# Performance work log

Measured on AMD Instinct MI355X. Metric: run time of the kernel, lower is better.

The kernel has to match this reference:

```python
import jax, jax.numpy as jnp
import numpy as np

BITS = 4
IN_F = 4096
OUT_F = 4096
NUMVALS = 200000
TOPX = 10
B, S = 4, 2048


def setup_inputs() -> dict:
    key = jax.random.key(0)
    ks = jax.random.split(key, 9)
    x = jax.random.normal(ks[0], (B, S, IN_F), dtype=jnp.float32)
    qweight = jax.random.randint(ks[1], (IN_F // 32 * BITS, OUT_F),
                                 jnp.iinfo(jnp.int32).min, jnp.iinfo(jnp.int32).max,
                                 dtype=jnp.int32)
    lookup_table = jax.random.normal(ks[2], (OUT_F, 2 ** BITS), dtype=jnp.float32) * 0.02
    bias = jax.random.normal(ks[3], (OUT_F,), dtype=jnp.float32) * 0.01
    rows = jnp.sort(jax.random.randint(ks[4], (OUT_F + 1,), 0, NUMVALS, dtype=jnp.int32))
    rows = rows.at[0].set(0).at[-1].set(NUMVALS)  # valid CSR row pointers
    cols = jax.random.randint(ks[5], (NUMVALS,), 0, IN_F, dtype=jnp.int32)
    vals = jax.random.normal(ks[6], (NUMVALS,), dtype=jnp.float32) * 0.02
    full_rows = jax.random.normal(ks[7], (IN_F, TOPX), dtype=jnp.float32) * 0.02
    full_row_indices = (jnp.arange(TOPX, dtype=jnp.int32) * (OUT_F // TOPX))
    return {"x": x, "qweight": qweight, "lookup_table": lookup_table, "bias": bias,
            "rows": rows, "cols": cols, "vals": vals,
            "full_rows": full_rows, "full_row_indices": full_row_indices}


def _dequant(qweight, lookup_table):
    # unpack 4-bit codes packed along infeatures into each int32 word
    per_word = 32 // BITS
    shifts = (jnp.arange(per_word, dtype=jnp.int32) * BITS)
    codes = (qweight[:, None, :] >> shifts[None, :, None]) & ((1 << BITS) - 1)
    codes = codes.reshape(-1, qweight.shape[1])  # (IN_F, OUT_F)
    # per-output-channel LUT gather: W[i, j] = lut[j, codes[i, j]]
    return jnp.take_along_axis(lookup_table.T, codes, axis=0)  # (IN_F, OUT_F)


def reference(x, qweight, lookup_table, bias, rows, cols, vals, full_rows, full_row_indices):
    w = _dequant(qweight, lookup_table)  # (IN_F, OUT_F) float32
    # CSR sparse outlier correction (row pointers over output channels)
    nnz = vals.shape[0]
    row_ids = jnp.searchsorted(rows, jnp.arange(nnz, dtype=jnp.int32), side="right") - 1
    w = w.at[cols, row_ids].add(vals)
    # topX dense outlier channels
    w = w.at[:, full_row_indices].add(full_rows)
    tokens = x.reshape(-1, x.shape[-1])  # (B*S, IN_F)
    y = tokens @ w + bias
    return y.reshape(x.shape[:-1] + (w.shape[1],))
```

## Files before the change

### kernel.cpp

```cpp
#include <hip/hip_runtime.h>
#include <hip/hip_bf16.h>
#include <stdint.h>

#define IN_F 4096
#define OUT_F 4096
#define MTOK 8192
#define TOPX_N 10
#define NUMVALS 200000
#define CSR_BLOCKS ((NUMVALS + 255) / 256)
#define CVT_BLOCKS ((MTOK * IN_F / 8) / 256)

typedef __bf16 bf16x8 __attribute__((ext_vector_type(8)));
typedef float f32x4 __attribute__((ext_vector_type(4)));

__device__ __forceinline__ void gld_lds16(const void* g, void* l) {
    __builtin_amdgcn_global_load_lds((const __attribute__((address_space(1))) void*)g,
                                     (__attribute__((address_space(3))) void*)l, 16, 0, 0);
}

__global__ __launch_bounds__(256) void k_dequant(const int* __restrict__ qw,
                                                 const float* __restrict__ lut,
                                                 __bf16* __restrict__ Wt) {
    __shared__ int qs[64 * 65];
    __shared__ float ls[64 * 16];
    const int b = blockIdx.x;
    const int jc = (b & 63) * 64;
    const int wc = (b >> 6) * 64;
    const int t = threadIdx.x;

    {
        float4 v = *(const float4*)(lut + (size_t)(jc + (t >> 2)) * 16 + (t & 3) * 4);
        *(float4*)(ls + (t >> 2) * 16 + (t & 3) * 4) = v;
    }
#pragma unroll
    for (int p = 0; p < 4; ++p) {
        int idx = t + p * 256;
        int row = idx >> 4;
        int c4 = (idx & 15) * 4;
        int4 v = *(const int4*)(qw + (size_t)(wc + row) * OUT_F + jc + c4);
        int base = row * 65 + c4;
        qs[base] = v.x; qs[base + 1] = v.y; qs[base + 2] = v.z; qs[base + 3] = v.w;
    }
    __syncthreads();

    const int wave = t >> 6, lane = t & 63;
#pragma unroll
    for (int i = 0; i < 16; ++i) {
        const int c = wave * 16 + i;
        const unsigned q = (unsigned)qs[lane * 65 + c];
        const float* lp = ls + c * 16;
        bf16x8 v;
#pragma unroll
        for (int e = 0; e < 8; ++e) v[e] = (__bf16)lp[(q >> (4 * e)) & 15];
        *(bf16x8*)(Wt + (size_t)(jc + c) * IN_F + (size_t)(wc + lane) * 8) = v;
    }
}

__device__ __forceinline__ void bf16_cas_add(__bf16* Wt, size_t elem, float v) {
    unsigned* wp = (unsigned*)Wt + (elem >> 1);
    unsigned sh = (unsigned)(elem & 1) * 16;
    unsigned old = *wp, assumed;
    do {
        assumed = old;
        union { unsigned u; float f; } cv;
        cv.u = ((assumed >> sh) & 0xFFFFu) << 16;
        __bf16 nb = (__bf16)(cv.f + v);
        unsigned nh = *(unsigned short*)&nb;
        unsigned newv = (assumed & ~(0xFFFFu << sh)) | ((unsigned)nh << sh);
        old = atomicCAS(wp, assumed, newv);
    } while (old != assumed);
}

__global__ __launch_bounds__(256) void k_prep(const float* __restrict__ x,
                                              __bf16* __restrict__ xb,
                                              const int* __restrict__ rows,
                                              const int* __restrict__ cols,
                                              const float* __restrict__ vals,
                                              const float* __restrict__ fr,
                                              const int* __restrict__ fri,
                                              __bf16* __restrict__ Wt) {
    const int b = blockIdx.x;
    if (b < CVT_BLOCKS) {
        size_t t = (size_t)b * 256 + threadIdx.x;
        const float4* p = (const float4*)x + 2 * t;
        float4 a = p[0], c = p[1];
        bf16x8 v;
        v[0] = (__bf16)a.x; v[1] = (__bf16)a.y; v[2] = (__bf16)a.z; v[3] = (__bf16)a.w;
        v[4] = (__bf16)c.x; v[5] = (__bf16)c.y; v[6] = (__bf16)c.z; v[7] = (__bf16)c.w;
        ((bf16x8*)xb)[t] = v;
    } else if (b < CVT_BLOCKS + CSR_BLOCKS) {
        int n = (b - CVT_BLOCKS) * 256 + threadIdx.x;
        if (n >= NUMVALS) return;
        int lo = 0, hi = OUT_F + 1;
        while (lo < hi) {
            int mid = (lo + hi) >> 1;
            if (rows[mid] <= n) lo = mid + 1; else hi = mid;
        }
        int r = lo - 1;
        bf16_cas_add(Wt, (size_t)r * IN_F + cols[n], vals[n]);
    } else {
        int i = (b - CVT_BLOCKS - CSR_BLOCKS) * 256 + threadIdx.x;
        if (i >= IN_F) return;
#pragma unroll
        for (int t = 0; t < TOPX_N; ++t) {
            int j = fri[t];
            bf16_cas_add(Wt, (size_t)j * IN_F + i, fr[(size_t)i * TOPX_N + t]);
        }
    }
}

#define BK_G 32
#define NKT (IN_F / BK_G)
#define TILE_BYTES 16384
#define MFMA_ __builtin_amdgcn_mfma_f32_16x16x32_bf16

__global__ __launch_bounds__(512, 2) void k_gemm(const __bf16* __restrict__ A,
                                                 const __bf16* __restrict__ Bt,
                                                 const float* __restrict__ bias,
                                                 float* __restrict__ C) {
    __shared__ __align__(1024) char smem[4][2][TILE_BYTES];

    const int tid = threadIdx.x;
    const int wave = tid >> 6, lane = tid & 63;
    const int wm = wave >> 2, wn = wave & 3;

    const int bid = blockIdx.x;
    const int swz = (bid & 7) * 64 + (bid >> 3);
    const int n0 = (swz & 15) * 256;
    const int m0 = (swz >> 4) * 256;

    const int q = lane & 7, g = (lane >> 3) & 3, rh = lane >> 5;
    const int rloc = ((5 * (q - g + 8)) & 7) + 8 * rh;
    const int w0 = wave * 2;

    const char* gA0 = (const char*)(A  + (size_t)(m0 + w0 * 16 + rloc) * IN_F) + g * 16;
    const char* gA1 = gA0 + 16 * IN_F * 2;
    const char* gB0 = (const char*)(Bt + (size_t)(n0 + w0 * 16 + rloc) * IN_F) + g * 16;
    const char* gB1 = gB0 + 16 * IN_F * 2;
    char* lA = (char*)smem[0][0] + w0 * 1024;
    char* lB = (char*)smem[0][1] + w0 * 1024;

    const int lrow = lane & 15, kk = lane >> 4;
    const int rdc = ((5 * lrow + kk) & 7) * 16 + kk * 128 + (lrow >> 3) * 512;
    const int rdA = wm * 8192 + rdc;
    const int rdB = wn * 4096 + rdc;

#define STAGE(boff, koff) do {                               \
        gld_lds16(gA0 + (koff), lA + (boff));                \
        gld_lds16(gA1 + (koff), lA + (boff) + 1024);         \
        gld_lds16(gB0 + (koff), lB + (boff));                \
        gld_lds16(gB1 + (koff), lB + (boff) + 1024);         \
    } while (0)

#define COMPUTE(boff) do {                                                                     \
        const char* pA = (const char*)smem[0][0] + (boff) + rdA;                               \
        const char* pB = (const char*)smem[0][1] + (boff) + rdB;                               \
        bf16x8 bfr[4], af0[4], af1[4];                                                         \
        _Pragma("unroll") for (int n = 0; n < 4; ++n) bfr[n] = *(const bf16x8*)(pB + n * 1024);\
        _Pragma("unroll") for (int m = 0; m < 4; ++m) af0[m] = *(const bf16x8*)(pA + m * 1024);\
        _Pragma("unroll") for (int m = 0; m < 4; ++m) af1[m] = *(const bf16x8*)(pA + 4096 + m * 1024);\
        __builtin_amdgcn_s_setprio(1);                                                         \
        _Pragma("unroll") for (int m = 0; m < 4; ++m)                                          \
            _Pragma("unroll") for (int n = 0; n < 4; ++n)                                      \
                acc[m][n] = MFMA_(af0[m], bfr[n], acc[m][n], 0, 0, 0);                         \
        _Pragma("unroll") for (int m = 0; m < 4; ++m)                                          \
            _Pragma("unroll") for (int n = 0; n < 4; ++n)                                      \
                acc[m + 4][n] = MFMA_(af1[m], bfr[n], acc[m + 4][n], 0, 0, 0);                 \
        __builtin_amdgcn_s_setprio(0);                                                         \
    } while (0)

    f32x4 acc[8][4] = {};

    STAGE(0, 0);
    STAGE(32768, 64);
    STAGE(65536, 128);

    int cboff = 0, sboff = 98304;
    for (int t = 0; t < NKT - 2; ++t) {
        asm volatile("s_waitcnt vmcnt(8)" ::: "memory");
        __builtin_amdgcn_s_barrier();
        asm volatile("" ::: "memory");
        if (t + 3 < NKT) STAGE(sboff, (t + 3) * 64);
        COMPUTE(cboff);
        cboff = cboff == 98304 ? 0 : cboff + 32768;
        sboff = sboff == 98304 ? 0 : sboff + 32768;
    }
    asm volatile("s_waitcnt vmcnt(4)" ::: "memory");
    __builtin_amdgcn_s_barrier();
    asm volatile("" ::: "memory");
    COMPUTE(cboff);
    cboff = cboff == 98304 ? 0 : cboff + 32768;
    asm volatile("s_waitcnt vmcnt(0)" ::: "memory");
    __builtin_amdgcn_s_barrier();
    asm volatile("" ::: "memory");
    COMPUTE(cboff);

    const int m0w = m0 + wm * 128;
    const int n0w = n0 + wn * 64;
#pragma unroll
    for (int n = 0; n < 4; ++n) {
        const int col = n0w + n * 16 + lrow;
        const float bj = bias[col];
#pragma unroll
        for (int m = 0; m < 8; ++m) {
            const int row = m0w + m * 16 + kk * 4;
#pragma unroll
            for (int r = 0; r < 4; ++r)
                C[(size_t)(row + r) * OUT_F + col] = acc[m][n][r] + bj;
        }
    }
#undef STAGE
#undef COMPUTE
}

extern "C" void kernel_launch(void* const* d_in, const int* in_sizes, int n_in,
                              void* d_out, int out_size, void* d_ws, size_t ws_size,
                              hipStream_t stream) {
    const float* x         = (const float*)d_in[0];
    const int*   qweight   = (const int*)d_in[1];
    const float* lut       = (const float*)d_in[2];
    const float* bias      = (const float*)d_in[3];
    const int*   rows      = (const int*)d_in[4];
    const int*   cols      = (const int*)d_in[5];
    const float* vals      = (const float*)d_in[6];
    const float* full_rows = (const float*)d_in[7];
    const int*   fri       = (const int*)d_in[8];
    float* out = (float*)d_out;

    __bf16* Wt = (__bf16*)d_ws;
    __bf16* xb = (__bf16*)((char*)d_ws + (size_t)OUT_F * IN_F * 2);

    k_dequant<<<dim3(64 * 8), 256, 0, stream>>>(qweight, lut, Wt);
    k_prep<<<dim3(CVT_BLOCKS + CSR_BLOCKS + IN_F / 256), 256, 0, stream>>>(
        x, xb, rows, cols, vals, full_rows, fri, Wt);
    k_gemm<<<dim3((OUT_F / 256) * (MTOK / 256)), 512, 0, stream>>>(xb, Wt, bias, out);
}
```

Measured before the change: 533.4 us.

## Double-buffer LDS fragment reads in registers to overlap with MFMA compute

Restructures the GEMM main loop into a software-pipelined ping-pong: the LDS fragment reads for the next k-tile go into a second register set while MFMAs run on the current set. Scheduling barriers pin this order. The loop is manually unrolled by two with explicit waitcnt and barrier placement, and the tail is rewritten. The aim is to hide LDS read latency behind matrix math, at the cost of doubling the fragment registers, which may pressure occupancy at two blocks per CU.

```diff
diff --git a/kernel.cpp b/kernel.cpp
--- a/kernel.cpp
+++ b/kernel.cpp
@@ -113,12 +113,18 @@
 #define NKT (IN_F / BK_G)
 #define TILE_BYTES 16384
 #define MFMA_ __builtin_amdgcn_mfma_f32_16x16x32_bf16
+#define SB0 __builtin_amdgcn_sched_barrier(0)
+#define VMC4  asm volatile("s_waitcnt vmcnt(4)" ::: "memory")
+#define VMC0  asm volatile("s_waitcnt vmcnt(0)" ::: "memory")
+#define BARF  do { __builtin_amdgcn_s_barrier(); asm volatile("" ::: "memory"); } while (0)
+#define ROT(x) ((x) == 98304 ? 0 : (x) + 32768)
 
 __global__ __launch_bounds__(512, 2) void k_gemm(const __bf16* __restrict__ A,
                                                  const __bf16* __restrict__ Bt,
                                                  const float* __restrict__ bias,
                                                  float* __restrict__ C) {
     __shared__ __align__(1024) char smem[4][2][TILE_BYTES];
+    char* const sm = (char*)smem;
 
     const int tid = threadIdx.x;
     const int wave = tid >> 6, lane = tid & 63;
@@ -143,7 +149,7 @@
     const int lrow = lane & 15, kk = lane >> 4;
     const int rdc = ((5 * lrow + kk) & 7) * 16 + kk * 128 + (lrow >> 3) * 512;
     const int rdA = wm * 8192 + rdc;
-    const int rdB = wn * 4096 + rdc;
+    const int rdB = 16384 + wn * 4096 + rdc;
 
 #define STAGE(boff, koff) do {                               \
         gld_lds16(gA0 + (koff), lA + (boff));                \
@@ -152,48 +158,56 @@
         gld_lds16(gB1 + (koff), lB + (boff) + 1024);         \
     } while (0)
 
-#define COMPUTE(boff) do {                                                                     \
-        const char* pA = (const char*)smem[0][0] + (boff) + rdA;                               \
-        const char* pB = (const char*)smem[0][1] + (boff) + rdB;                               \
-        bf16x8 bfr[4], af0[4], af1[4];                                                         \
-        _Pragma("unroll") for (int n = 0; n < 4; ++n) bfr[n] = *(const bf16x8*)(pB + n * 1024);\
-        _Pragma("unroll") for (int m = 0; m < 4; ++m) af0[m] = *(const bf16x8*)(pA + m * 1024);\
-        _Pragma("unroll") for (int m = 0; m < 4; ++m) af1[m] = *(const bf16x8*)(pA + 4096 + m * 1024);\
-        __builtin_amdgcn_s_setprio(1);                                                         \
-        _Pragma("unroll") for (int m = 0; m < 4; ++m)                                          \
-            _Pragma("unroll") for (int n = 0; n < 4; ++n)                                      \
-                acc[m][n] = MFMA_(af0[m], bfr[n], acc[m][n], 0, 0, 0);                         \
-        _Pragma("unroll") for (int m = 0; m < 4; ++m)                                          \
-            _Pragma("unroll") for (int n = 0; n < 4; ++n)                                      \
-                acc[m + 4][n] = MFMA_(af1[m], bfr[n], acc[m + 4][n], 0, 0, 0);                 \
-        __builtin_amdgcn_s_setprio(0);                                                         \
+#define RD(af_, bf_, boff) do {                                                  \
+        const char* pA = sm + (boff) + rdA;                                      \
+        const char* pB = sm + (boff) + rdB;                                      \
+        _Pragma("unroll") for (int n = 0; n < 4; ++n)                            \
+            bf_[n] = *(const bf16x8*)(pB + n * 1024);                            \
+        _Pragma("unroll") for (int m = 0; m < 8; ++m)                            \
+            af_[m] = *(const bf16x8*)(pA + m * 1024);                            \
     } while (0)
 
+#define CMP(af_, bf_) do {                                                       \
+        __builtin_amdgcn_s_setprio(1);                                           \
+        _Pragma("unroll") for (int m = 0; m < 8; ++m)                            \
+            _Pragma("unroll") for (int n = 0; n < 4; ++n)                        \
+                acc[m][n] = MFMA_(af_[m], bf_[n], acc[m][n], 0, 0, 0);           \
+        __builtin_amdgcn_s_setprio(0);                                           \
+    } while (0)
+
     f32x4 acc[8][4] = {};
+    bf16x8 afA[8], bfA[4], afB[8], bfB[4];
 
     STAGE(0, 0);
     STAGE(32768, 64);
     STAGE(65536, 128);
-
-    int cboff = 0, sboff = 98304;
-    for (int t = 0; t < NKT - 2; ++t) {
-        asm volatile("s_waitcnt vmcnt(8)" ::: "memory");
-        __builtin_amdgcn_s_barrier();
-        asm volatile("" ::: "memory");
-        if (t + 3 < NKT) STAGE(sboff, (t + 3) * 64);
-        COMPUTE(cboff);
-        cboff = cboff == 98304 ? 0 : cboff + 32768;
-        sboff = sboff == 98304 ? 0 : sboff + 32768;
-    }
-    asm volatile("s_waitcnt vmcnt(4)" ::: "memory");
-    __builtin_amdgcn_s_barrier();
-    asm volatile("" ::: "memory");
-    COMPUTE(cboff);
-    cboff = cboff == 98304 ? 0 : cboff + 32768;
-    asm volatile("s_waitcnt vmcnt(0)" ::: "memory");
-    __builtin_amdgcn_s_barrier();
-    asm volatile("" ::: "memory");
-    COMPUTE(cboff);
+    asm volatile("s_waitcnt vmcnt(8)" ::: "memory");
+    BARF;
+    RD(afA, bfA, 0);
+    SB0;
+
+    int rboff = 32768;
+    int sboff = 98304;
+
+    for (int h = 0; h < 63; ++h) {
+        VMC4; BARF;
+        STAGE(sboff, (2 * h + 3) * 64);
+        RD(afB, bfB, rboff);
+        SB0;
+        CMP(afA, bfA);
+        rboff = ROT(rboff); sboff = ROT(sboff);
+        VMC4; BARF;
+        if (h < 62) STAGE(sboff, (2 * h + 4) * 64);
+        RD(afA, bfA, rboff);
+        SB0;
+        CMP(afB, bfB);
+        rboff = ROT(rboff); sboff = ROT(sboff);
+    }
+    VMC0; BARF;
+    RD(afB, bfB, rboff);
+    SB0;
+    CMP(afA, bfA);
+    CMP(afB, bfB);
 
     const int m0w = m0 + wm * 128;
     const int n0w = n0 + wn * 64;
@@ -210,7 +224,8 @@
         }
     }
 #undef STAGE
-#undef COMPUTE
+#undef RD
+#undef CMP
 }
 
 extern "C" void kernel_launch(void* const* d_in, const int* in_sizes, int n_in,
```

New measurement: 543.0 us. Within noise of the previous version (+1.8%).
